# Kernel optimization log

Measured on AMD Instinct MI355X. Metric: run time of the kernel, lower is better.

Reference implementation:

```python
import jax, jax.numpy as jnp
import numpy as np
from functools import partial

FS = 30.0
CUTOFF = 3.3
ORDER = 5
PADLEN = 18  # scipy filtfilt default: 3 * max(len(a), len(b)) = 3 * 6


def butter_lowpass_np(order, Wn):
    """Digital Butterworth lowpass (b, a), matching scipy.signal.butter."""
    # analog prototype poles (buttap)
    m = np.arange(-order + 1, order, 2)
    p = -np.exp(1j * np.pi * m / (2 * order))
    k = 1.0
    # pre-warp frequency (scipy uses internal fs = 2.0)
    fs = 2.0
    warped = 2 * fs * np.tan(np.pi * Wn / fs)
    p = warped * p
    k = k * warped ** order
    # bilinear transform
    fs2 = 2 * fs
    p_z = (fs2 + p) / (fs2 - p)
    z_z = -np.ones(order)
    k_z = k * np.real(1.0 / np.prod(fs2 - p))
    b = k_z * np.real(np.poly(z_z))
    a = np.real(np.poly(p_z))
    return b.astype(np.float64), a.astype(np.float64)


def lfilter_zi_np(b, a):
    """Steady-state initial conditions, matching scipy.signal.lfilter_zi."""
    n = len(a)
    comp = np.zeros((n - 1, n - 1))
    comp[0, :] = -a[1:] / a[0]
    if n > 2:
        comp[1:, :-1] = np.eye(n - 2)
    B = b[1:] - a[1:] * b[0]
    return np.linalg.solve(np.eye(n - 1) - comp.T, B)


def lfilter(b, a, x, zi):
    """Direct-form II transposed IIR filter along a 1-D signal via lax.scan."""
    def step(z, xt):
        y = b[0] * xt + z[0]
        z_shift = jnp.concatenate([z[1:], jnp.zeros(1, z.dtype)])
        z_new = b[1:] * xt + z_shift - a[1:] * y
        return z_new, y
    _, y = jax.lax.scan(step, zi, x)
    return y


def filtfilt_1d(b, a, zi, x):
    """Zero-phase filtering with odd-extension padding (scipy filtfilt defaults)."""
    left = 2 * x[0] - x[PADLEN:0:-1]
    right = 2 * x[-1] - x[-2:-(PADLEN + 2):-1]
    ext = jnp.concatenate([left, x, right])
    y = lfilter(b, a, ext, zi * ext[0])
    y = lfilter(b, a, y[::-1], zi * y[-1])[::-1]
    return y[PADLEN:-PADLEN]


def setup_inputs() -> dict:
    key = jax.random.key(0)
    x = jax.random.normal(key, (4096, 8192), dtype=jnp.float32)
    Wn = CUTOFF / (FS / 2.0)
    b_np, a_np = butter_lowpass_np(ORDER, Wn)
    zi_np = lfilter_zi_np(b_np, a_np)
    return {
        "x": x,
        "b": jnp.asarray(b_np, dtype=jnp.float32),
        "a": jnp.asarray(a_np, dtype=jnp.float32),
        "zi": jnp.asarray(zi_np, dtype=jnp.float32),
    }


def reference(x, b, a, zi):
    # batched zero-phase Butterworth lowpass, [batch, length] -> [batch, length]
    return jax.vmap(partial(filtfilt_1d, b, a, zi))(x)
```

## Files before the change

kernel.cpp:

```cpp
#include <hip/hip_runtime.h>


#define NN   8192
#define PADL 18
#define LC   32
#define WC   32
#define TPB  256
#define CH   33
#define LDSZ (256 * CH + PADL)

__device__ __forceinline__ int pidx(int j) { return j + (j >> 5); }

#define STEP(xv) do {                               \
    float y_ = fmaf(b0, (xv), z0);                  \
    z0 = fmaf(na1, y_, fmaf(b1, (xv), z1));         \
    z1 = fmaf(na2, y_, fmaf(b2, (xv), z2));         \
    z2 = fmaf(na3, y_, fmaf(b3, (xv), z3));         \
    z3 = fmaf(na4, y_, fmaf(b4, (xv), z4));         \
    z4 = fmaf(na5, y_, b5 * (xv));                  \
    yv = y_;                                        \
} while (0)

__global__ __launch_bounds__(TPB, 4) void GREEN_62869731278967_filtfilt(
    const float* __restrict__ x,
    const float* __restrict__ bc,
    const float* __restrict__ ac,
    const float* __restrict__ zc,
    float* __restrict__ out)
{
    __shared__ float lds[LDSZ];
    const int row = blockIdx.x;
    const int tid = threadIdx.x;
    const float* xr   = x   + (size_t)row * NN;
    float*       outr = out + (size_t)row * NN;

    const float b0 = bc[0], b1 = bc[1], b2 = bc[2], b3 = bc[3], b4 = bc[4], b5 = bc[5];
    const float na1 = -ac[1], na2 = -ac[2], na3 = -ac[3], na4 = -ac[4], na5 = -ac[5];
    const float zi0 = zc[0], zi1 = zc[1], zi2 = zc[2], zi3 = zc[3], zi4 = zc[4];

#pragma unroll
    for (int q = 0; q < NN / (TPB * 4); ++q) {
        int i = (q * TPB + tid) * 4;
        float4 v = *reinterpret_cast<const float4*>(xr + i);
        int p = pidx(i);
        lds[p + 0] = v.x;
        lds[p + 1] = v.y;
        lds[p + 2] = v.z;
        lds[p + 3] = v.w;
    }
    __syncthreads();

    const float x0 = lds[0];
    const float xN = lds[pidx(NN - 1)];

    float yreg[LC];
    float ytail[PADL];
    {
        float z0, z1, z2, z3, z4, yv;
        if (tid == 0) {
            float v0 = 2.f * x0 - lds[pidx(PADL)];
            z0 = zi0 * v0; z1 = zi1 * v0; z2 = zi2 * v0; z3 = zi3 * v0; z4 = zi4 * v0;
#pragma unroll 3
            for (int t = 0; t < PADL; ++t) {
                float v = 2.f * x0 - lds[pidx(PADL - t)];
                STEP(v);
            }
        } else {
            const float* p = &lds[(tid - 1) * CH];
            float v0 = p[0];
            z0 = zi0 * v0; z1 = zi1 * v0; z2 = zi2 * v0; z3 = zi3 * v0; z4 = zi4 * v0;
#pragma unroll 4
            for (int i = 0; i < WC; ++i) STEP(p[i]);
        }
        {
            const float* p = &lds[tid * CH];
#pragma unroll
            for (int i = 0; i < LC; ++i) { STEP(p[i]); yreg[i] = yv; }
        }
        if (tid == TPB - 1) {
#pragma unroll 3
            for (int i = 0; i < PADL; ++i) {
                float v = 2.f * xN - lds[pidx(NN - 2 - i)];
                STEP(v);
                ytail[i] = yv;
            }
        }
    }
    __syncthreads();

    {
        float* p = &lds[tid * CH];
#pragma unroll
        for (int i = 0; i < LC; ++i) p[i] = yreg[i];
    }
    if (tid == TPB - 1) {
#pragma unroll 3
        for (int i = 0; i < PADL; ++i) lds[256 * CH + i] = ytail[i];
    }
    __syncthreads();

    {
        float z0, z1, z2, z3, z4, yv;
        if (tid == TPB - 1) {
            float u0 = lds[256 * CH + PADL - 1];
            z0 = zi0 * u0; z1 = zi1 * u0; z2 = zi2 * u0; z3 = zi3 * u0; z4 = zi4 * u0;
#pragma unroll 3
            for (int s = 0; s < PADL; ++s) {
                float v = lds[256 * CH + PADL - 1 - s];
                STEP(v);
            }
        } else {
            const float* p = &lds[(tid + 1) * CH];
            float u0 = p[LC - 1];
            z0 = zi0 * u0; z1 = zi1 * u0; z2 = zi2 * u0; z3 = zi3 * u0; z4 = zi4 * u0;
#pragma unroll 4
            for (int i = 0; i < WC; ++i) STEP(p[LC - 1 - i]);
        }
        float freg[LC];
        {
            const float* p = &lds[tid * CH];
#pragma unroll
            for (int i = 0; i < LC; ++i) { STEP(p[LC - 1 - i]); freg[LC - 1 - i] = yv; }
        }
#pragma unroll
        for (int q = 0; q < LC / 4; ++q) {
            float4 v;
            v.x = freg[4 * q + 0];
            v.y = freg[4 * q + 1];
            v.z = freg[4 * q + 2];
            v.w = freg[4 * q + 3];
            *reinterpret_cast<float4*>(outr + tid * LC + 4 * q) = v;
        }
    }
}

extern "C" void kernel_launch(void* const* d_in, const int* in_sizes, int n_in,
                              void* d_out, int out_size, void* d_ws, size_t ws_size,
                              hipStream_t stream) {
    const float* x  = (const float*)d_in[0];
    const float* b  = (const float*)d_in[1];
    const float* a  = (const float*)d_in[2];
    const float* zi = (const float*)d_in[3];
    float* out = (float*)d_out;
    const int rows = in_sizes[0] / NN;
    GREEN_62869731278967_filtfilt<<<rows, TPB, 0, stream>>>(x, b, a, zi, out);
}
```

Baseline: 65.91 us.

## Use XOR-swizzled transposed LDS layout and reuse register chunk in backward pass

Replaces the padded row-major LDS layout (stride 33) with a transposed layout where element i of chunk c lives at i*256 + swizzled c. Reads by all threads at the same i then hit consecutive banks, and the LDS array shrinks to exactly 8192 floats. The backward pass now reads its own chunk from yreg registers and the tail from ytail instead of re-reading LDS. Launch bounds rise to 5 blocks per CU and the warm-up loops are fully unrolled. The costs are heavier register pressure under the tighter bound and a more complex global-to-LDS scatter pattern.

```diff
diff --git a/kernel.cpp b/kernel.cpp
--- a/kernel.cpp
+++ b/kernel.cpp
@@ -4,12 +4,11 @@
 #define NN   8192
 #define PADL 18
 #define LC   32
-#define WC   32
 #define TPB  256
-#define CH   33
-#define LDSZ (256 * CH + PADL)
 
-__device__ __forceinline__ int pidx(int j) { return j + (j >> 5); }
+__device__ __forceinline__ int xw(int c, int i) {
+    return (i << 8) + (c ^ (((i >> 2) & 7) << 2));
+}
 
 #define STEP(xv) do {                               \
     float y_ = fmaf(b0, (xv), z0);                  \
@@ -21,14 +20,14 @@
     yv = y_;                                        \
 } while (0)
 
-__global__ __launch_bounds__(TPB, 4) void GREEN_62869731278967_filtfilt(
+__global__ __launch_bounds__(TPB, 5) void GREEN_62869731278967_filtfilt(
     const float* __restrict__ x,
     const float* __restrict__ bc,
     const float* __restrict__ ac,
     const float* __restrict__ zc,
     float* __restrict__ out)
 {
-    __shared__ float lds[LDSZ];
+    __shared__ float lds[NN];
     const int row = blockIdx.x;
     const int tid = threadIdx.x;
     const float* xr   = x   + (size_t)row * NN;
@@ -38,49 +37,47 @@
     const float na1 = -ac[1], na2 = -ac[2], na3 = -ac[3], na4 = -ac[4], na5 = -ac[5];
     const float zi0 = zc[0], zi1 = zc[1], zi2 = zc[2], zi3 = zc[3], zi4 = zc[4];
 
+    {
+        const int Abase = ((tid & 7) << 10) + ((tid >> 3) ^ ((tid & 7) << 2));
 #pragma unroll
-    for (int q = 0; q < NN / (TPB * 4); ++q) {
-        int i = (q * TPB + tid) * 4;
-        float4 v = *reinterpret_cast<const float4*>(xr + i);
-        int p = pidx(i);
-        lds[p + 0] = v.x;
-        lds[p + 1] = v.y;
-        lds[p + 2] = v.z;
-        lds[p + 3] = v.w;
+        for (int q = 0; q < 8; ++q) {
+            float4 v = *reinterpret_cast<const float4*>(xr + (q << 10) + (tid << 2));
+            lds[Abase + (q << 5) + 0]   = v.x;
+            lds[Abase + (q << 5) + 256] = v.y;
+            lds[Abase + (q << 5) + 512] = v.z;
+            lds[Abase + (q << 5) + 768] = v.w;
+        }
     }
     __syncthreads();
 
-    const float x0 = lds[0];
-    const float xN = lds[pidx(NN - 1)];
+    const float x0 = lds[xw(0, 0)];
+    const float xN = lds[xw(255, 31)];
 
     float yreg[LC];
     float ytail[PADL];
     {
         float z0, z1, z2, z3, z4, yv;
         if (tid == 0) {
-            float v0 = 2.f * x0 - lds[pidx(PADL)];
+            float v0 = 2.f * x0 - lds[xw(0, PADL)];
             z0 = zi0 * v0; z1 = zi1 * v0; z2 = zi2 * v0; z3 = zi3 * v0; z4 = zi4 * v0;
-#pragma unroll 3
+#pragma unroll
             for (int t = 0; t < PADL; ++t) {
-                float v = 2.f * x0 - lds[pidx(PADL - t)];
+                float v = 2.f * x0 - lds[xw(0, PADL - t)];
                 STEP(v);
             }
         } else {
-            const float* p = &lds[(tid - 1) * CH];
-            float v0 = p[0];
+            const int cp = tid - 1;
+            float v0 = lds[xw(cp, 0)];
             z0 = zi0 * v0; z1 = zi1 * v0; z2 = zi2 * v0; z3 = zi3 * v0; z4 = zi4 * v0;
-#pragma unroll 4
-            for (int i = 0; i < WC; ++i) STEP(p[i]);
+#pragma unroll
+            for (int i = 0; i < LC; ++i) STEP(lds[xw(cp, i)]);
         }
-        {
-            const float* p = &lds[tid * CH];
 #pragma unroll
-            for (int i = 0; i < LC; ++i) { STEP(p[i]); yreg[i] = yv; }
-        }
+        for (int i = 0; i < LC; ++i) { STEP(lds[xw(tid, i)]); yreg[i] = yv; }
         if (tid == TPB - 1) {
-#pragma unroll 3
+#pragma unroll
             for (int i = 0; i < PADL; ++i) {
-                float v = 2.f * xN - lds[pidx(NN - 2 - i)];
+                float v = 2.f * xN - lds[xw(255, 30 - i)];
                 STEP(v);
                 ytail[i] = yv;
             }
@@ -88,40 +85,27 @@
     }
     __syncthreads();
 
-    {
-        float* p = &lds[tid * CH];
 #pragma unroll
-        for (int i = 0; i < LC; ++i) p[i] = yreg[i];
-    }
-    if (tid == TPB - 1) {
-#pragma unroll 3
-        for (int i = 0; i < PADL; ++i) lds[256 * CH + i] = ytail[i];
-    }
+    for (int i = 0; i < LC; ++i) lds[xw(tid, i)] = yreg[i];
     __syncthreads();
 
     {
         float z0, z1, z2, z3, z4, yv;
         if (tid == TPB - 1) {
-            float u0 = lds[256 * CH + PADL - 1];
+            float u0 = ytail[PADL - 1];
             z0 = zi0 * u0; z1 = zi1 * u0; z2 = zi2 * u0; z3 = zi3 * u0; z4 = zi4 * u0;
-#pragma unroll 3
-            for (int s = 0; s < PADL; ++s) {
-                float v = lds[256 * CH + PADL - 1 - s];
-                STEP(v);
-            }
+#pragma unroll
+            for (int s = 0; s < PADL; ++s) STEP(ytail[PADL - 1 - s]);
         } else {
-            const float* p = &lds[(tid + 1) * CH];
-            float u0 = p[LC - 1];
+            const int cn = tid + 1;
+            float u0 = lds[xw(cn, LC - 1)];
             z0 = zi0 * u0; z1 = zi1 * u0; z2 = zi2 * u0; z3 = zi3 * u0; z4 = zi4 * u0;
-#pragma unroll 4
-            for (int i = 0; i < WC; ++i) STEP(p[LC - 1 - i]);
+#pragma unroll
+            for (int i = 0; i < LC; ++i) STEP(lds[xw(cn, LC - 1 - i)]);
         }
         float freg[LC];
-        {
-            const float* p = &lds[tid * CH];
 #pragma unroll
-            for (int i = 0; i < LC; ++i) { STEP(p[LC - 1 - i]); freg[LC - 1 - i] = yv; }
-        }
+        for (int i = 0; i < LC; ++i) { STEP(yreg[LC - 1 - i]); freg[LC - 1 - i] = yv; }
 #pragma unroll
         for (int q = 0; q < LC / 4; ++q) {
             float4 v;
```

Measured after the change: 63.24 us. 1.04x faster.
